# Optimization experiments

Hardware: AMD Instinct MI355X
Metric: run time of the kernel (lower is better)

Reference implementation:

```python
import jax, jax.numpy as jnp
import numpy as np
from jax import lax

B, T, I, H, L = 64, 256, 512, 1024, 2


def setup_inputs() -> dict:
    key = jax.random.key(0)
    ks = jax.random.split(key, 6)
    s = 0.05  # small init scale for numerical stability
    return {
        "x": jax.random.normal(ks[0], (B, T, I), dtype=jnp.float32),
        "h0": jnp.zeros((L, B, H), dtype=jnp.float32),
        "c0": jnp.zeros((L, B, H), dtype=jnp.float32),
        "W_ih_0": jax.random.normal(ks[1], (I, 4 * H), dtype=jnp.float32) * s,
        "W_hh_0": jax.random.normal(ks[2], (H, 4 * H), dtype=jnp.float32) * s,
        "b_0": jnp.zeros((4 * H,), dtype=jnp.float32),
        "W_ih_1": jax.random.normal(ks[3], (H, 4 * H), dtype=jnp.float32) * s,
        "W_hh_1": jax.random.normal(ks[4], (H, 4 * H), dtype=jnp.float32) * s,
        "b_1": jnp.zeros((4 * H,), dtype=jnp.float32),
    }


def _lstm_layer(x_tbd, h0, c0, W_ih, W_hh, b):
    """x_tbd: [T, B, in]; returns ([T, B, H], h_T, c_T). Standard (Zaremba) LSTM cell."""
    def step(carry, xt):
        h, c = carry
        gates = xt @ W_ih + h @ W_hh + b  # [B, 4H]
        i, f, g, o = jnp.split(gates, 4, axis=-1)
        i = jax.nn.sigmoid(i)
        f = jax.nn.sigmoid(f)
        g = jnp.tanh(g)
        o = jax.nn.sigmoid(o)
        c_new = f * c + i * g
        h_new = o * jnp.tanh(c_new)
        return (h_new, c_new), h_new

    (h_T, c_T), ys = lax.scan(step, (h0, c0), x_tbd)
    return ys, h_T, c_T


def reference(x, h0, c0, W_ih_0, W_hh_0, b_0, W_ih_1, W_hh_1, b_1):
    # x: [B, T, I] batch-first as in the torch module; scan over time.
    xt = jnp.swapaxes(x, 0, 1)  # [T, B, I]
    weights = [(W_ih_0, W_hh_0, b_0), (W_ih_1, W_hh_1, b_1)]
    hs, cs = [], []
    values = xt
    for l in range(L):
        W_ih, W_hh, b = weights[l]
        values, h_T, c_T = _lstm_layer(values, h0[l], c0[l], W_ih, W_hh, b)
        hs.append(h_T)
        cs.append(c_T)
    outputs = jnp.swapaxes(values, 0, 1)  # [B, T, H]
    return outputs, jnp.stack(hs, 0), jnp.stack(cs, 0)
```

## Files before the change

kernel.cpp:

```cpp
#include <hip/hip_runtime.h>
#include <hip/hip_bf16.h>

typedef __attribute__((ext_vector_type(8))) short short8;
typedef __attribute__((ext_vector_type(4))) float f32x4;
typedef __attribute__((ext_vector_type(4))) int int4v;

constexpr int BB = 64;
constexpr int TT = 256;
constexpr int II = 512;
constexpr int HH = 1024;

constexpr int NBLK = 256;
constexpr int NTHR = 512;

constexpr int HTILE = (HH / 8) * BB * 8;
constexpr int XTILE = (II / 8) * BB * 8;
constexpr int RING = 8;

constexpr size_t OFF_FLAGS = 0;
constexpr size_t OFF_WIH0T = 4096;
constexpr size_t OFF_WHH0T = OFF_WIH0T + (size_t)4096 * 512 * 2;
constexpr size_t OFF_WIH1T = OFF_WHH0T + (size_t)4096 * 1024 * 2;
constexpr size_t OFF_WHH1T = OFF_WIH1T + (size_t)4096 * 1024 * 2;
constexpr size_t OFF_XT    = OFF_WHH1T + (size_t)4096 * 1024 * 2;
constexpr size_t OFF_H0D   = OFF_XT + (size_t)TT * XTILE * 2;
constexpr size_t OFF_H1D   = OFF_H0D + (size_t)RING * HTILE * 2;

__device__ __forceinline__ float sigmoid_(float x) {
  return 1.f / (1.f + __expf(-x));
}
__device__ __forceinline__ float tanh_(float x) {
  float ax = fabsf(x);
  float e = __expf(-2.f * ax);
  float t = (1.f - e) / (1.f + e);
  return copysignf(t, x);
}

__global__ void zero_flags(int* f) { f[blockIdx.x * 256 + threadIdx.x] = 0; }

__global__ void transpose_to_bf16(const float* __restrict__ src,
                                  __hip_bfloat16* __restrict__ dst,
                                  int K, int N) {
  __shared__ float tile[64][65];
  const int n0 = blockIdx.x * 64;
  const int k0 = blockIdx.y * 64;
  const int tx = threadIdx.x & 63;
  const int ty = threadIdx.x >> 6;
#pragma unroll
  for (int i = 0; i < 64; i += 4)
    tile[ty + i][tx] = src[(size_t)(k0 + ty + i) * N + n0 + tx];
  __syncthreads();
#pragma unroll
  for (int i = 0; i < 64; i += 4) {
    const int n = ty + i;
    dst[(size_t)(n0 + n) * K + k0 + tx] = __float2bfloat16(tile[tx][n]);
  }
}

__global__ void tile_x(const float* __restrict__ x, __hip_bfloat16* __restrict__ xt) {
  const int t = blockIdx.x;
  const int k = threadIdx.x;
  __hip_bfloat16* o = xt + (size_t)t * XTILE;
  for (int b = 0; b < BB; ++b) {
    float v = x[((size_t)b * TT + t) * II + k];
    o[(k >> 3) * (BB * 8) + b * 8 + (k & 7)] = __float2bfloat16(v);
  }
}

__global__ void init_h(const float* __restrict__ h0, __hip_bfloat16* h0d, __hip_bfloat16* h1d) {
  const int idx = blockIdx.x * 256 + threadIdx.x;
  const int l = idx >> 16;
  const int b = (idx >> 10) & 63;
  const int j = idx & 1023;
  __hip_bfloat16 v = __float2bfloat16(h0[idx]);
  __hip_bfloat16* dst = l ? h1d : h0d;
  dst[(j >> 3) * (BB * 8) + b * 8 + (j & 7)] = v;
}

template <int LAYER>
__device__ __forceinline__ int chunk_kg(int wave, int c) {
  if constexpr (LAYER == 0)
    return (c < 2) ? (wave * 2 + c) * 32 : 512 + (wave * 4 + (c - 2)) * 32;
  else
    return (c < 4) ? (wave * 4 + c) * 32 : 1024 + (wave * 4 + (c - 4)) * 32;
}

template <int KI, int KW, int CA, int LAYER>
__device__ __forceinline__ void scan_impl(
    const __hip_bfloat16* __restrict__ xsrc,
    const __hip_bfloat16* __restrict__ WiT,
    const __hip_bfloat16* __restrict__ WhT,
    const float* __restrict__ bias,
    const float* __restrict__ c0_in,
    __hip_bfloat16* h0d, __hip_bfloat16* h1d,
    float* __restrict__ out, int* flags, f32x4 (*part)[2][4][64],
    int bhalf, int jbase) {
  const int tid = threadIdx.x;
  const int wave = tid >> 6;
  const int lane = tid & 63;
  const int cc = lane & 15;
  const int lrow = lane >> 4;
  constexpr int NB = KW - CA;

  short8 Bf[KW][4];
#pragma unroll
  for (int c = 0; c < KW; ++c) {
    const int kg = chunk_kg<LAYER>(wave, c) + lrow * 8;
#pragma unroll
    for (int g = 0; g < 4; ++g) {
      const int gcol = g * HH + jbase + cc;
      const __hip_bfloat16* p;
      if (kg < KI) p = WiT + (size_t)gcol * KI + kg;
      else         p = WhT + (size_t)gcol * HH + (kg - KI);
      Bf[c][g] = *(const short8*)p;
    }
  }

  const int ejl = tid & 15;
  const int ebl = tid >> 4;
  const int ej = jbase + ejl;
  const int eb = bhalf * 32 + ebl;
  const int pm = ebl >> 4, psub = (ebl >> 2) & 3, pr = ebl & 3;
  const int rdbase = pm * 1024 + (psub * 16 + ejl) * 4 + pr;
  const float bi = bias[ej];
  const float bf_ = bias[HH + ej];
  const float bg = bias[2 * HH + ej];
  const float bo = bias[3 * HH + ej];
  float cst = c0_in[(size_t)LAYER * BB * HH + (size_t)eb * HH + ej];

  const int* fquad = flags + lane * 4;

  for (int tau = 0; tau < TT + 2; ++tau) {
    const bool active = (LAYER == 0) ? (tau < TT) : (tau >= 2);
    const int p = (LAYER == 0) ? tau : tau - 2;

    const __hip_bfloat16* px;
    const __hip_bfloat16* ph;
    __hip_bfloat16* hout;
    if constexpr (LAYER == 0) {
      px = xsrc + (size_t)p * XTILE;
      ph = h0d + (size_t)(p & (RING - 1)) * HTILE;
      hout = h0d + (size_t)((p + 1) & (RING - 1)) * HTILE;
    } else {
      px = h0d + (size_t)((p + 1) & (RING - 1)) * HTILE;
      ph = h1d + (size_t)(p & (RING - 1)) * HTILE;
      hout = h1d + (size_t)((p + 1) & (RING - 1)) * HTILE;
    }

    f32x4 acc[2][4] = {};
    short8 abuf[4][2];

    auto issue_chunk = [&](int c, short8* dst) {
      const int kg = chunk_kg<LAYER>(wave, c);
      const __hip_bfloat16* ab;
      int kc;
      if (kg < KI) { ab = px; kc = (kg >> 3) + lrow; }
      else         { ab = ph; kc = ((kg - KI) >> 3) + lrow; }
#pragma unroll
      for (int m = 0; m < 2; ++m) {
        const __hip_bfloat16* ptr =
            ab + (size_t)kc * (BB * 8) + (size_t)(bhalf * 32 + m * 16 + cc) * 8;
        asm volatile("global_load_dwordx4 %0, %1, off" : "=v"(dst[m]) : "v"(ptr));
      }
    };

    if (active) {
#pragma unroll
      for (int c = 0; c < CA; ++c) issue_chunk(c, abuf[c]);
    }

    if (tau > 0 && wave == 0) {
      for (;;) {
        int4v v;
        asm volatile("global_load_dwordx4 %0, %1, off sc0 sc1\n\t"
                     "s_waitcnt vmcnt(0)"
                     : "=v"(v) : "v"(fquad) : "memory");
        int mn = min(min(v.x, v.y), min(v.z, v.w));
        if (__all(mn >= tau)) break;
        __builtin_amdgcn_s_sleep(2);
      }
    }

    if (active) {
      asm volatile("s_waitcnt vmcnt(0)" ::: "memory");
      __builtin_amdgcn_sched_barrier(0);
#pragma unroll
      for (int c = 0; c < CA; ++c)
#pragma unroll
        for (int m = 0; m < 2; ++m)
#pragma unroll
          for (int g = 0; g < 4; ++g)
            acc[m][g] = __builtin_amdgcn_mfma_f32_16x16x32_bf16(
                abuf[c][m], Bf[c][g], acc[m][g], 0, 0, 0);
    }

    __syncthreads();
    if (wave == 0)
      __builtin_amdgcn_fence(__ATOMIC_ACQUIRE, "agent");
    __syncthreads();

    if (active) {
#pragma unroll
      for (int c = 0; c < NB; ++c) issue_chunk(CA + c, abuf[c]);
#pragma unroll
      for (int c = 0; c < NB; ++c) {
        const int vm = 2 * (NB - 1 - c);
        if (vm == 6)      asm volatile("s_waitcnt vmcnt(6)" ::: "memory");
        else if (vm == 4) asm volatile("s_waitcnt vmcnt(4)" ::: "memory");
        else if (vm == 2) asm volatile("s_waitcnt vmcnt(2)" ::: "memory");
        else              asm volatile("s_waitcnt vmcnt(0)" ::: "memory");
        __builtin_amdgcn_sched_barrier(0);
#pragma unroll
        for (int m = 0; m < 2; ++m)
#pragma unroll
          for (int g = 0; g < 4; ++g)
            acc[m][g] = __builtin_amdgcn_mfma_f32_16x16x32_bf16(
                abuf[c][m], Bf[CA + c][g], acc[m][g], 0, 0, 0);
      }

#pragma unroll
      for (int m = 0; m < 2; ++m)
#pragma unroll
        for (int g = 0; g < 4; ++g)
          part[wave][m][g][lane] = acc[m][g];
      __syncthreads();

      const float* pp = (const float*)part;
      float s0 = 0.f, s1 = 0.f, s2 = 0.f, s3 = 0.f;
#pragma unroll
      for (int w = 0; w < 8; ++w) {
        s0 += pp[w * 2048 + 0 * 256 + rdbase];
        s1 += pp[w * 2048 + 1 * 256 + rdbase];
        s2 += pp[w * 2048 + 2 * 256 + rdbase];
        s3 += pp[w * 2048 + 3 * 256 + rdbase];
      }
      float iv = sigmoid_(s0 + bi);
      float fv = sigmoid_(s1 + bf_);
      float gv = tanh_(s2 + bg);
      float ov = sigmoid_(s3 + bo);
      float cn = fv * cst + iv * gv;
      cst = cn;
      float hv = ov * tanh_(cn);
      __hip_bfloat16 hb = __float2bfloat16(hv);
      unsigned short hu = *reinterpret_cast<unsigned short*>(&hb);
      unsigned pu = (unsigned)__shfl_xor((int)hu, 1);
      if ((tid & 1) == 0) {
        uint32_t packed = (uint32_t)hu | ((pu & 0xffffu) << 16);
        uint32_t* hq = (uint32_t*)hout;
        __hip_atomic_store(hq + (ej >> 3) * 256 + eb * 4 + ((ej & 7) >> 1), packed,
                           __ATOMIC_RELAXED, __HIP_MEMORY_SCOPE_AGENT);
      }
      asm volatile("s_waitcnt vmcnt(0)" ::: "memory");
      __syncthreads();
      if (tid == 0)
        __hip_atomic_store(&flags[blockIdx.x], tau + 1, __ATOMIC_RELAXED, __HIP_MEMORY_SCOPE_AGENT);
      if constexpr (LAYER == 1)
        out[((size_t)eb * TT + p) * HH + ej] = hv;
      if (p == TT - 1) {
        out[(size_t)BB * TT * HH + (size_t)LAYER * BB * HH + (size_t)eb * HH + ej] = hv;
        out[(size_t)BB * TT * HH + (size_t)2 * BB * HH + (size_t)LAYER * BB * HH + (size_t)eb * HH + ej] = cn;
      }
    } else {
      if (tid == 0)
        __hip_atomic_store(&flags[blockIdx.x], tau + 1, __ATOMIC_RELAXED, __HIP_MEMORY_SCOPE_AGENT);
    }
  }
}

__global__ __launch_bounds__(NTHR, 2) void lstm_scan(
    const __hip_bfloat16* __restrict__ xt,
    const __hip_bfloat16* __restrict__ Wih0T, const __hip_bfloat16* __restrict__ Whh0T,
    const __hip_bfloat16* __restrict__ Wih1T, const __hip_bfloat16* __restrict__ Whh1T,
    const float* __restrict__ b0, const float* __restrict__ b1,
    const float* __restrict__ c0_in,
    __hip_bfloat16* h0d, __hip_bfloat16* h1d,
    float* __restrict__ out, int* flags) {
  __shared__ f32x4 part[8][2][4][64];
  const int blk = blockIdx.x;
  const int jslot = blk & 63;
  const int bhalf = (blk >> 6) & 1;
  const int jbase = jslot * 16;
  if ((blk >> 7) == 0)
    scan_impl<512, 6, 2, 0>(xt, Wih0T, Whh0T, b0, c0_in, h0d, h1d, out, flags, part, bhalf, jbase);
  else
    scan_impl<1024, 8, 4, 1>(nullptr, Wih1T, Whh1T, b1, c0_in, h0d, h1d, out, flags, part, bhalf, jbase);
}

extern "C" void kernel_launch(void* const* d_in, const int* in_sizes, int n_in,
                              void* d_out, int out_size, void* d_ws, size_t ws_size,
                              hipStream_t stream) {
  (void)in_sizes; (void)n_in; (void)out_size; (void)ws_size;
  const float* x    = (const float*)d_in[0];
  const float* h0   = (const float*)d_in[1];
  const float* c0   = (const float*)d_in[2];
  const float* Wih0 = (const float*)d_in[3];
  const float* Whh0 = (const float*)d_in[4];
  const float* b0   = (const float*)d_in[5];
  const float* Wih1 = (const float*)d_in[6];
  const float* Whh1 = (const float*)d_in[7];
  const float* b1   = (const float*)d_in[8];
  float* out = (float*)d_out;
  char* ws = (char*)d_ws;

  int* flags = (int*)(ws + OFF_FLAGS);
  __hip_bfloat16* wih0t = (__hip_bfloat16*)(ws + OFF_WIH0T);
  __hip_bfloat16* whh0t = (__hip_bfloat16*)(ws + OFF_WHH0T);
  __hip_bfloat16* wih1t = (__hip_bfloat16*)(ws + OFF_WIH1T);
  __hip_bfloat16* whh1t = (__hip_bfloat16*)(ws + OFF_WHH1T);
  __hip_bfloat16* xtl   = (__hip_bfloat16*)(ws + OFF_XT);
  __hip_bfloat16* h0d   = (__hip_bfloat16*)(ws + OFF_H0D);
  __hip_bfloat16* h1d   = (__hip_bfloat16*)(ws + OFF_H1D);

  zero_flags<<<2, 256, 0, stream>>>(flags);
  transpose_to_bf16<<<dim3(64, 8),  256, 0, stream>>>(Wih0, wih0t, 512, 4096);
  transpose_to_bf16<<<dim3(64, 16), 256, 0, stream>>>(Whh0, whh0t, 1024, 4096);
  transpose_to_bf16<<<dim3(64, 16), 256, 0, stream>>>(Wih1, wih1t, 1024, 4096);
  transpose_to_bf16<<<dim3(64, 16), 256, 0, stream>>>(Whh1, whh1t, 1024, 4096);
  tile_x<<<TT, 512, 0, stream>>>(x, xtl);
  init_h<<<512, 256, 0, stream>>>(h0, h0d, h1d);
  lstm_scan<<<NBLK, NTHR, 0, stream>>>(xtl, wih0t, whh0t, wih1t, whh1t,
                                       b0, b1, c0, h0d, h1d, out, flags);
}
```

Baseline: 1.668 ms.

## Split grid barrier per batch half and drop a redundant block sync

Flag slots are remapped so each batch half has its own group of 128 flags covering both layers. Each block now polls only the 128 flags of its own half with dwordx2 loads instead of all 256 flags. This relaxes the global barrier into two independent half-grid barriers, since batch halves never exchange hidden state. A __syncthreads before the acquire fence is removed, and an extra vmcnt wait after the output stores keeps outstanding stores from colliding with the next step's counted loads.

Result: faster. 1.521 ms (-8.8%).

```diff
diff --git a/kernel.cpp b/kernel.cpp
--- a/kernel.cpp
+++ b/kernel.cpp
@@ -3,7 +3,7 @@
 
 typedef __attribute__((ext_vector_type(8))) short short8;
 typedef __attribute__((ext_vector_type(4))) float f32x4;
-typedef __attribute__((ext_vector_type(4))) int int4v;
+typedef __attribute__((ext_vector_type(2))) int int2v;
 
 constexpr int BB = 64;
 constexpr int TT = 256;
@@ -94,7 +94,7 @@
     const float* __restrict__ c0_in,
     __hip_bfloat16* h0d, __hip_bfloat16* h1d,
     float* __restrict__ out, int* flags, f32x4 (*part)[2][4][64],
-    int bhalf, int jbase) {
+    int bhalf, int jbase, int fslot) {
   const int tid = threadIdx.x;
   const int wave = tid >> 6;
   const int lane = tid & 63;
@@ -128,7 +128,7 @@
   const float bo = bias[3 * HH + ej];
   float cst = c0_in[(size_t)LAYER * BB * HH + (size_t)eb * HH + ej];
 
-  const int* fquad = flags + lane * 4;
+  const int* fpair = flags + bhalf * 128 + lane * 2;
 
   for (int tau = 0; tau < TT + 2; ++tau) {
     const bool active = (LAYER == 0) ? (tau < TT) : (tau >= 2);
@@ -171,11 +171,11 @@
 
     if (tau > 0 && wave == 0) {
       for (;;) {
-        int4v v;
-        asm volatile("global_load_dwordx4 %0, %1, off sc0 sc1\n\t"
+        int2v v;
+        asm volatile("global_load_dwordx2 %0, %1, off sc0 sc1\n\t"
                      "s_waitcnt vmcnt(0)"
-                     : "=v"(v) : "v"(fquad) : "memory");
-        int mn = min(min(v.x, v.y), min(v.z, v.w));
+                     : "=v"(v) : "v"(fpair) : "memory");
+        int mn = min(v.x, v.y);
         if (__all(mn >= tau)) break;
         __builtin_amdgcn_s_sleep(2);
       }
@@ -194,8 +194,7 @@
                 abuf[c][m], Bf[c][g], acc[m][g], 0, 0, 0);
     }
 
-    __syncthreads();
-    if (wave == 0)
+    if (tau > 0 && wave == 0)
       __builtin_amdgcn_fence(__ATOMIC_ACQUIRE, "agent");
     __syncthreads();
 
@@ -253,16 +252,17 @@
       asm volatile("s_waitcnt vmcnt(0)" ::: "memory");
       __syncthreads();
       if (tid == 0)
-        __hip_atomic_store(&flags[blockIdx.x], tau + 1, __ATOMIC_RELAXED, __HIP_MEMORY_SCOPE_AGENT);
+        __hip_atomic_store(&flags[fslot], tau + 1, __ATOMIC_RELAXED, __HIP_MEMORY_SCOPE_AGENT);
       if constexpr (LAYER == 1)
         out[((size_t)eb * TT + p) * HH + ej] = hv;
       if (p == TT - 1) {
         out[(size_t)BB * TT * HH + (size_t)LAYER * BB * HH + (size_t)eb * HH + ej] = hv;
         out[(size_t)BB * TT * HH + (size_t)2 * BB * HH + (size_t)LAYER * BB * HH + (size_t)eb * HH + ej] = cn;
       }
+      asm volatile("s_waitcnt vmcnt(0)" ::: "memory");
     } else {
       if (tid == 0)
-        __hip_atomic_store(&flags[blockIdx.x], tau + 1, __ATOMIC_RELAXED, __HIP_MEMORY_SCOPE_AGENT);
+        __hip_atomic_store(&flags[fslot], tau + 1, __ATOMIC_RELAXED, __HIP_MEMORY_SCOPE_AGENT);
     }
   }
 }
@@ -279,11 +279,13 @@
   const int blk = blockIdx.x;
   const int jslot = blk & 63;
   const int bhalf = (blk >> 6) & 1;
+  const int layer = blk >> 7;
   const int jbase = jslot * 16;
-  if ((blk >> 7) == 0)
-    scan_impl<512, 6, 2, 0>(xt, Wih0T, Whh0T, b0, c0_in, h0d, h1d, out, flags, part, bhalf, jbase);
+  const int fslot = bhalf * 128 + layer * 64 + jslot;
+  if (layer == 0)
+    scan_impl<512, 6, 2, 0>(xt, Wih0T, Whh0T, b0, c0_in, h0d, h1d, out, flags, part, bhalf, jbase, fslot);
   else
-    scan_impl<1024, 8, 4, 1>(nullptr, Wih1T, Whh1T, b1, c0_in, h0d, h1d, out, flags, part, bhalf, jbase);
+    scan_impl<1024, 8, 4, 1>(nullptr, Wih1T, Whh1T, b1, c0_in, h0d, h1d, out, flags, part, bhalf, jbase, fslot);
 }
 
 extern "C" void kernel_launch(void* const* d_in, const int* in_sizes, int n_in,
```
